# Performance work log

Measured on AMD Instinct MI355X. Metric: run time of the kernel, lower is better.

The kernel has to match this reference:

```python
import jax, jax.numpy as jnp
import numpy as np

ALPHA = 1.1
COMMISSION = 0.05
BET_PCT = 0.02
B = 4_194_304
T = 6  # num traps


def setup_inputs() -> dict:
    key = jax.random.key(0)
    k1, k2, k3, k4 = jax.random.split(key, 4)
    predicted_probs = jax.random.uniform(k1, (B, T), dtype=jnp.float32)
    true_winners = (jax.random.uniform(k2, (B, T)) > 0.8).astype(jnp.float32)
    market_odds = jax.random.uniform(k3, (B, T), dtype=jnp.float32) * 10.0
    invalid = jax.random.uniform(k4, (B, 1)) < 0.1
    market_odds = jnp.where(invalid, 0.0, market_odds)
    return {"predicted_probs": predicted_probs, "true_winners": true_winners,
            "market_odds": market_odds}


def reference(predicted_probs, true_winners, market_odds):
    batch_size = predicted_probs.shape[0]
    payout_scale = BET_PCT * (1.0 - COMMISSION)

    has_valid_odds = jnp.any(market_odds > 0, axis=1)  # [B]
    # expected profit per dog; zero for races without valid odds
    ep = (market_odds * ALPHA * predicted_probs - 1.0) * payout_scale  # [B,T]
    ep = jnp.where(has_valid_odds[:, None], ep, 0.0)

    best_idx = jnp.argmax(ep, axis=1)  # [B], first-max like torch
    best_ep = jnp.take_along_axis(ep, best_idx[:, None], axis=1)[:, 0]  # [B]
    should_bet = (best_ep > 0) & has_valid_odds  # [B]

    # actual profits (not part of the differentiable loss; tracked as metrics)
    odds_b = jnp.take_along_axis(market_odds, best_idx[:, None], axis=1)[:, 0]
    win_b = jnp.take_along_axis(true_winners, best_idx[:, None], axis=1)[:, 0]
    win_profit = (odds_b * ALPHA * BET_PCT - BET_PCT) * (1.0 - COMMISSION)
    lose_profit = -BET_PCT * (1.0 - COMMISSION)
    actual_profits = jnp.where(should_bet,
                               jnp.where(win_b > 0.5, win_profit, lose_profit),
                               0.0)

    any_bet = jnp.any(should_bet)
    sum_bet_ep = jnp.sum(jnp.where(should_bet, best_ep, 0.0))
    fallback = -jnp.mean(jnp.max(predicted_probs, axis=1)) * 0.1
    total_expected_profit = jnp.where(any_bet, sum_bet_ep, fallback)
    loss = -total_expected_profit / batch_size

    batch_profit = jnp.sum(actual_profits)
    num_bets = jnp.sum(should_bet.astype(jnp.int32))
    return loss, batch_profit, num_bets
```

## Files before the change

### kernel.cpp

```cpp
#include <hip/hip_runtime.h>
#include <math.h>


constexpr int T = 6;
constexpr int NTHR = 256;
constexpr int NBLK = 1024;
constexpr int CHUNK_PAIRS = 256;
constexpr int F4_PER_ARR = CHUNK_PAIRS * 3;

typedef float f4 __attribute__((ext_vector_type(4)));

__device__ __forceinline__ void stage16(const f4* g, f4* l) {
    __builtin_amdgcn_global_load_lds(
        (const __attribute__((address_space(1))) void*)g,
        (__attribute__((address_space(3))) void*)l,
        16, 0, 0);
}

__global__ __launch_bounds__(NTHR) void betting_stage1(
    const f4* __restrict__ probs4,
    const f4* __restrict__ winners4,
    const f4* __restrict__ odds4,
    double* __restrict__ partials,
    int npairs)
{
    __shared__ f4 lp[F4_PER_ARR];
    __shared__ f4 lo[F4_PER_ARR];
    __shared__ f4 lw[F4_PER_ARR];

    const float ALPHA = 1.1f;
    const float BET = 0.02f;
    const float KEEP = 0.95f;
    const float PS = BET * KEEP;

    double s_ep = 0.0, s_profit = 0.0, s_maxp = 0.0;
    int cnt = 0;

    const int t = threadIdx.x;
    const int nchunks = npairs / CHUNK_PAIRS;

    for (int c = blockIdx.x; c < nchunks; c += gridDim.x) {
        const size_t gb = (size_t)c * F4_PER_ARR;
        #pragma unroll
        for (int k = 0; k < 3; ++k) {
            const int idx = k * NTHR + t;
            stage16(probs4   + gb + idx, &lp[idx]);
            stage16(odds4    + gb + idx, &lo[idx]);
            stage16(winners4 + gb + idx, &lw[idx]);
        }
        __syncthreads();

        const float* rp = (const float*)lp + t * 12;
        const float* ro = (const float*)lo + t * 12;
        const float* rw = (const float*)lw + t * 12;
        f4 P0 = *(const f4*)(rp);  f4 P1 = *(const f4*)(rp + 4);  f4 P2 = *(const f4*)(rp + 8);
        f4 O0 = *(const f4*)(ro);  f4 O1 = *(const f4*)(ro + 4);  f4 O2 = *(const f4*)(ro + 8);
        float p[12] = {P0.x, P0.y, P0.z, P0.w, P1.x, P1.y, P1.z, P1.w, P2.x, P2.y, P2.z, P2.w};
        float o[12] = {O0.x, O0.y, O0.z, O0.w, O1.x, O1.y, O1.z, O1.w, O2.x, O2.y, O2.z, O2.w};

        #pragma unroll
        for (int rr = 0; rr < 2; ++rr) {
            const int off = rr * T;
            bool valid = false;
            float maxp = p[off];
            float best_ep = -INFINITY;
            float best_odds = 0.0f;
            int bestj = 0;
            #pragma unroll
            for (int j = 0; j < T; ++j) {
                const float oj = o[off + j];
                const float pj = p[off + j];
                valid |= (oj > 0.0f);
                maxp = fmaxf(maxp, pj);
                const float ep = (oj * ALPHA * pj - 1.0f) * PS;
                if (ep > best_ep) { best_ep = ep; best_odds = oj; bestj = j; }
            }
            s_maxp += (double)maxp;
            const bool bet = valid && (best_ep > 0.0f);
            const float wbest = rw[off + bestj];
            s_ep += bet ? (double)best_ep : 0.0;
            cnt += bet ? 1 : 0;
            const float profit = (wbest > 0.5f)
                ? (best_odds * ALPHA * BET - BET) * KEEP
                : -BET * KEEP;
            s_profit += bet ? (double)profit : 0.0;
        }
        __syncthreads();
    }

    for (int i = nchunks * CHUNK_PAIRS + blockIdx.x * NTHR + t;
         i < npairs; i += gridDim.x * NTHR) {
        const size_t b = (size_t)i * 3;
        f4 P0 = probs4[b], P1 = probs4[b + 1], P2 = probs4[b + 2];
        f4 O0 = odds4[b],  O1 = odds4[b + 1],  O2 = odds4[b + 2];
        f4 W0 = winners4[b], W1 = winners4[b + 1], W2 = winners4[b + 2];
        float p[12] = {P0.x, P0.y, P0.z, P0.w, P1.x, P1.y, P1.z, P1.w, P2.x, P2.y, P2.z, P2.w};
        float o[12] = {O0.x, O0.y, O0.z, O0.w, O1.x, O1.y, O1.z, O1.w, O2.x, O2.y, O2.z, O2.w};
        float w[12] = {W0.x, W0.y, W0.z, W0.w, W1.x, W1.y, W1.z, W1.w, W2.x, W2.y, W2.z, W2.w};
        #pragma unroll
        for (int rr = 0; rr < 2; ++rr) {
            const int off = rr * T;
            bool valid = false;
            float maxp = p[off];
            float best_ep = -INFINITY;
            float best_odds = 0.0f, best_win = 0.0f;
            #pragma unroll
            for (int j = 0; j < T; ++j) {
                const float oj = o[off + j];
                const float pj = p[off + j];
                valid |= (oj > 0.0f);
                maxp = fmaxf(maxp, pj);
                const float ep = (oj * ALPHA * pj - 1.0f) * PS;
                if (ep > best_ep) { best_ep = ep; best_odds = oj; best_win = w[off + j]; }
            }
            s_maxp += (double)maxp;
            const bool bet = valid && (best_ep > 0.0f);
            s_ep += bet ? (double)best_ep : 0.0;
            cnt += bet ? 1 : 0;
            const float profit = (best_win > 0.5f)
                ? (best_odds * ALPHA * BET - BET) * KEEP
                : -BET * KEEP;
            s_profit += bet ? (double)profit : 0.0;
        }
    }

    #pragma unroll
    for (int off = 32; off > 0; off >>= 1) {
        s_ep     += __shfl_down(s_ep, off);
        s_profit += __shfl_down(s_profit, off);
        s_maxp   += __shfl_down(s_maxp, off);
        cnt      += __shfl_down(cnt, off);
    }

    __shared__ double sm_ep[NTHR / 64];
    __shared__ double sm_pr[NTHR / 64];
    __shared__ double sm_mx[NTHR / 64];
    __shared__ int    sm_ct[NTHR / 64];
    const int lane = t & 63;
    const int wid  = t >> 6;
    if (lane == 0) {
        sm_ep[wid] = s_ep; sm_pr[wid] = s_profit; sm_mx[wid] = s_maxp; sm_ct[wid] = cnt;
    }
    __syncthreads();
    if (t == 0) {
        double t_ep = 0.0, t_pr = 0.0, t_mx = 0.0; int t_ct = 0;
        #pragma unroll
        for (int k = 0; k < NTHR / 64; ++k) {
            t_ep += sm_ep[k]; t_pr += sm_pr[k]; t_mx += sm_mx[k]; t_ct += sm_ct[k];
        }
        double* slot = partials + (size_t)blockIdx.x * 4;
        slot[0] = t_ep; slot[1] = t_pr; slot[2] = t_mx; slot[3] = (double)t_ct;
    }
}

__global__ __launch_bounds__(NTHR) void betting_stage2(
    const double* __restrict__ partials, float* __restrict__ out, int nblk, int B)
{
    double s_ep = 0.0, s_pr = 0.0, s_mx = 0.0, s_ct = 0.0;
    for (int i = threadIdx.x; i < nblk; i += blockDim.x) {
        const double* slot = partials + (size_t)i * 4;
        s_ep += slot[0]; s_pr += slot[1]; s_mx += slot[2]; s_ct += slot[3];
    }
    #pragma unroll
    for (int off = 32; off > 0; off >>= 1) {
        s_ep += __shfl_down(s_ep, off);
        s_pr += __shfl_down(s_pr, off);
        s_mx += __shfl_down(s_mx, off);
        s_ct += __shfl_down(s_ct, off);
    }
    __shared__ double sm[4][NTHR / 64];
    const int lane = threadIdx.x & 63;
    const int wid  = threadIdx.x >> 6;
    if (lane == 0) { sm[0][wid] = s_ep; sm[1][wid] = s_pr; sm[2][wid] = s_mx; sm[3][wid] = s_ct; }
    __syncthreads();
    if (threadIdx.x == 0) {
        double ep = 0.0, pr = 0.0, mx = 0.0, ct = 0.0;
        #pragma unroll
        for (int k = 0; k < NTHR / 64; ++k) { ep += sm[0][k]; pr += sm[1][k]; mx += sm[2][k]; ct += sm[3][k]; }
        bool any_bet = ct > 0.0;
        double total = any_bet ? ep : (-(mx / (double)B) * 0.1);
        out[0] = (float)(-total / (double)B);
        out[1] = (float)pr;
        out[2] = (float)ct;
    }
}

extern "C" void kernel_launch(void* const* d_in, const int* in_sizes, int n_in,
                              void* d_out, int out_size, void* d_ws, size_t ws_size,
                              hipStream_t stream) {
    const float* probs   = (const float*)d_in[0];
    const float* winners = (const float*)d_in[1];
    const float* odds    = (const float*)d_in[2];
    float* out = (float*)d_out;
    const int B = in_sizes[0] / T;
    const int npairs = B / 2;

    double* partials = (double*)d_ws;

    betting_stage1<<<NBLK, NTHR, 0, stream>>>(
        (const f4*)probs, (const f4*)winners, (const f4*)odds, partials, npairs);
    betting_stage2<<<1, NTHR, 0, stream>>>(partials, out, NBLK, B);
}
```

Before: 281.2 us.

## Replace block-wide LDS DMA staging with per-wave register prefetch pipeline

Each wave now owns a 64-pair chunk. It loads the next chunk into registers with nontemporal loads while it processes the current one, and uses a per-wave LDS slice only to transpose the data. This removes the block-wide __syncthreads barriers and the global_load_lds path, aiming to overlap memory latency with compute. In exchange it uses more registers for the double buffer and relies on wave-level LDS ordering with no explicit barrier between the LDS write and read.

After: 249.4 us. 1.13x faster.

```diff
diff --git a/kernel.cpp b/kernel.cpp
--- a/kernel.cpp
+++ b/kernel.cpp
@@ -5,16 +5,12 @@
 constexpr int T = 6;
 constexpr int NTHR = 256;
 constexpr int NBLK = 1024;
-constexpr int CHUNK_PAIRS = 256;
-constexpr int F4_PER_ARR = CHUNK_PAIRS * 3;
+constexpr int F4_PER_WAVE = 192;
 
 typedef float f4 __attribute__((ext_vector_type(4)));
 
-__device__ __forceinline__ void stage16(const f4* g, f4* l) {
-    __builtin_amdgcn_global_load_lds(
-        (const __attribute__((address_space(1))) void*)g,
-        (__attribute__((address_space(3))) void*)l,
-        16, 0, 0);
+__device__ __forceinline__ f4 ntload(const f4* p) {
+    return __builtin_nontemporal_load(p);
 }
 
 __global__ __launch_bounds__(NTHR) void betting_stage1(
@@ -24,9 +20,9 @@
     double* __restrict__ partials,
     int npairs)
 {
-    __shared__ f4 lp[F4_PER_ARR];
-    __shared__ f4 lo[F4_PER_ARR];
-    __shared__ f4 lw[F4_PER_ARR];
+    __shared__ f4 sP[4 * F4_PER_WAVE];
+    __shared__ f4 sO[4 * F4_PER_WAVE];
+    __shared__ f4 sW[4 * F4_PER_WAVE];
 
     const float ALPHA = 1.1f;
     const float BET = 0.02f;
@@ -37,22 +33,53 @@
     int cnt = 0;
 
     const int t = threadIdx.x;
-    const int nchunks = npairs / CHUNK_PAIRS;
-
-    for (int c = blockIdx.x; c < nchunks; c += gridDim.x) {
-        const size_t gb = (size_t)c * F4_PER_ARR;
-        #pragma unroll
-        for (int k = 0; k < 3; ++k) {
-            const int idx = k * NTHR + t;
-            stage16(probs4   + gb + idx, &lp[idx]);
-            stage16(odds4    + gb + idx, &lo[idx]);
-            stage16(winners4 + gb + idx, &lw[idx]);
-        }
-        __syncthreads();
-
-        const float* rp = (const float*)lp + t * 12;
-        const float* ro = (const float*)lo + t * 12;
-        const float* rw = (const float*)lw + t * 12;
+    const int lane = t & 63;
+    const int w = t >> 6;
+
+    f4* wp = sP + w * F4_PER_WAVE;
+    f4* wo = sO + w * F4_PER_WAVE;
+    f4* ww = sW + w * F4_PER_WAVE;
+
+    const long nchunks = npairs / 64;
+    const long waveId = (long)blockIdx.x * 4 + w;
+    const long waveStride = (long)gridDim.x * 4;
+
+    f4 A[3], Bv[3], Wv[3];
+    f4 A2[3], B2[3], W2[3];
+
+    long c = waveId;
+    if (c < nchunks) {
+        const size_t gb = (size_t)c * F4_PER_WAVE;
+        #pragma unroll
+        for (int r = 0; r < 3; ++r) {
+            A[r]  = ntload(probs4   + gb + r * 64 + lane);
+            Bv[r] = ntload(odds4    + gb + r * 64 + lane);
+            Wv[r] = ntload(winners4 + gb + r * 64 + lane);
+        }
+    }
+
+    while (c < nchunks) {
+        const long cn = c + waveStride;
+        if (cn < nchunks) {
+            const size_t gb = (size_t)cn * F4_PER_WAVE;
+            #pragma unroll
+            for (int r = 0; r < 3; ++r) {
+                A2[r] = ntload(probs4   + gb + r * 64 + lane);
+                B2[r] = ntload(odds4    + gb + r * 64 + lane);
+                W2[r] = ntload(winners4 + gb + r * 64 + lane);
+            }
+        }
+
+        #pragma unroll
+        for (int r = 0; r < 3; ++r) {
+            wp[r * 64 + lane] = A[r];
+            wo[r * 64 + lane] = Bv[r];
+            ww[r * 64 + lane] = Wv[r];
+        }
+
+        const float* rp = (const float*)wp + lane * 12;
+        const float* ro = (const float*)wo + lane * 12;
+        const float* rw = (const float*)ww + lane * 12;
         f4 P0 = *(const f4*)(rp);  f4 P1 = *(const f4*)(rp + 4);  f4 P2 = *(const f4*)(rp + 8);
         f4 O0 = *(const f4*)(ro);  f4 O1 = *(const f4*)(ro + 4);  f4 O2 = *(const f4*)(ro + 8);
         float p[12] = {P0.x, P0.y, P0.z, P0.w, P1.x, P1.y, P1.z, P1.w, P2.x, P2.y, P2.z, P2.w};
@@ -85,18 +112,21 @@
                 : -BET * KEEP;
             s_profit += bet ? (double)profit : 0.0;
         }
-        __syncthreads();
-    }
-
-    for (int i = nchunks * CHUNK_PAIRS + blockIdx.x * NTHR + t;
-         i < npairs; i += gridDim.x * NTHR) {
+
+        #pragma unroll
+        for (int r = 0; r < 3; ++r) { A[r] = A2[r]; Bv[r] = B2[r]; Wv[r] = W2[r]; }
+        c = cn;
+    }
+
+    for (long i = nchunks * 64 + (long)blockIdx.x * NTHR + t;
+         i < npairs; i += (long)gridDim.x * NTHR) {
         const size_t b = (size_t)i * 3;
         f4 P0 = probs4[b], P1 = probs4[b + 1], P2 = probs4[b + 2];
         f4 O0 = odds4[b],  O1 = odds4[b + 1],  O2 = odds4[b + 2];
-        f4 W0 = winners4[b], W1 = winners4[b + 1], W2 = winners4[b + 2];
+        f4 W0 = winners4[b], W1 = winners4[b + 1], W2f = winners4[b + 2];
         float p[12] = {P0.x, P0.y, P0.z, P0.w, P1.x, P1.y, P1.z, P1.w, P2.x, P2.y, P2.z, P2.w};
         float o[12] = {O0.x, O0.y, O0.z, O0.w, O1.x, O1.y, O1.z, O1.w, O2.x, O2.y, O2.z, O2.w};
-        float w[12] = {W0.x, W0.y, W0.z, W0.w, W1.x, W1.y, W1.z, W1.w, W2.x, W2.y, W2.z, W2.w};
+        float wv[12] = {W0.x, W0.y, W0.z, W0.w, W1.x, W1.y, W1.z, W1.w, W2f.x, W2f.y, W2f.z, W2f.w};
         #pragma unroll
         for (int rr = 0; rr < 2; ++rr) {
             const int off = rr * T;
@@ -111,7 +141,7 @@
                 valid |= (oj > 0.0f);
                 maxp = fmaxf(maxp, pj);
                 const float ep = (oj * ALPHA * pj - 1.0f) * PS;
-                if (ep > best_ep) { best_ep = ep; best_odds = oj; best_win = w[off + j]; }
+                if (ep > best_ep) { best_ep = ep; best_odds = oj; best_win = wv[off + j]; }
             }
             s_maxp += (double)maxp;
             const bool bet = valid && (best_ep > 0.0f);
@@ -136,10 +166,8 @@
     __shared__ double sm_pr[NTHR / 64];
     __shared__ double sm_mx[NTHR / 64];
     __shared__ int    sm_ct[NTHR / 64];
-    const int lane = t & 63;
-    const int wid  = t >> 6;
     if (lane == 0) {
-        sm_ep[wid] = s_ep; sm_pr[wid] = s_profit; sm_mx[wid] = s_maxp; sm_ct[wid] = cnt;
+        sm_ep[w] = s_ep; sm_pr[w] = s_profit; sm_mx[w] = s_maxp; sm_ct[w] = cnt;
     }
     __syncthreads();
     if (t == 0) {
```
